# Kernel optimization log

Hardware: AMD Instinct MI355X
Metric: run time of the kernel (lower is better)

The kernel has to match this reference:

```python
import jax, jax.numpy as jnp
import numpy as np
import math

B, S, D_MODEL, H, D_LATENT = 2, 2048, 2048, 16, 512
D_HEAD = D_MODEL // H


def setup_inputs() -> dict:
    key = jax.random.key(0)
    ks = jax.random.split(key, 6)
    s = lambda fan: 1.0 / math.sqrt(fan)
    return {
        "x": jax.random.normal(ks[0], (B, S, D_MODEL), dtype=jnp.float32),
        "W_q": jax.random.normal(ks[1], (D_MODEL, D_MODEL), dtype=jnp.float32) * s(D_MODEL),
        "W_down_kv": jax.random.normal(ks[2], (D_LATENT, D_MODEL), dtype=jnp.float32) * s(D_MODEL),
        "W_up_k": jax.random.normal(ks[3], (H, D_HEAD, D_LATENT), dtype=jnp.float32) * s(D_LATENT),
        "W_up_v": jax.random.normal(ks[4], (H, D_HEAD, D_LATENT), dtype=jnp.float32) * s(D_LATENT),
        "W_o": jax.random.normal(ks[5], (D_MODEL, D_MODEL), dtype=jnp.float32) * s(D_MODEL),
    }


def reference(x, W_q, W_down_kv, W_up_k, W_up_v, W_o):
    b, s_len, d_model = x.shape
    # Q: (B, H, S, Dh)
    Q = (x @ W_q.T).reshape(b, s_len, H, D_HEAD).transpose(0, 2, 1, 3)
    # latent KV: (B, S, d_latent)
    C_kv = x @ W_down_kv.T
    # per-head up-projections fused into one einsum: (B, H, S, Dh)
    K = jnp.einsum("bsl,hdl->bhsd", C_kv, W_up_k)
    V = jnp.einsum("bsl,hdl->bhsd", C_kv, W_up_v)
    scores = jnp.einsum("bhsd,bhtd->bhst", Q, K) / math.sqrt(D_HEAD)
    attn = jax.nn.softmax(scores, axis=-1)  # dropout p=0 / eval -> identity
    out = jnp.einsum("bhst,bhtd->bhsd", attn, V)
    out = out.transpose(0, 2, 1, 3).reshape(b, s_len, H * D_HEAD)
    return out @ W_o.T
```

## Files before the change

kernel.cpp:

```cpp
#include <hip/hip_runtime.h>
#include <hip/hip_bf16.h>

typedef __hip_bfloat16 bf16;
typedef __attribute__((ext_vector_type(8))) short short8v;
typedef __attribute__((ext_vector_type(4))) short short4v;
typedef __attribute__((ext_vector_type(4))) float f32x4;
typedef __attribute__((ext_vector_type(16))) float f32x16;
typedef __attribute__((ext_vector_type(4))) unsigned int uint4v;
typedef unsigned int u32;

#define MFMA_16x16x32(a, b, c) __builtin_amdgcn_mfma_f32_16x16x32_bf16((a), (b), (c), 0, 0, 0)
#define MFMA_32x32x16(a, b, c) __builtin_amdgcn_mfma_f32_32x32x16_bf16((a), (b), (c), 0, 0, 0)

constexpr int Bc = 2, Sc = 2048, DMc = 2048, Hc = 16, DLc = 512, DHc = 128;

__device__ __forceinline__ void gload_lds16(const bf16* g, void* lds) {
  __builtin_amdgcn_global_load_lds(
      (const __attribute__((address_space(1))) void*)g,
      (__attribute__((address_space(3))) void*)lds, 16, 0, 0);
}

__device__ __forceinline__ unsigned short bf16bits(float f) {
  return __builtin_bit_cast(unsigned short, __float2bfloat16(f));
}

struct CvtArgs {
  const float* src[6];
  bf16* dst[6];
  unsigned int cum[6];
  unsigned int total4;
};

__global__ __launch_bounds__(256) void cvt_all_kernel(CvtArgs a)
{
  unsigned int i = blockIdx.x * 256 + threadIdx.x;
  const unsigned int stride = gridDim.x * 256;
  for (; i < a.total4; i += stride) {
    int s = 0;
#pragma unroll
    for (int k = 1; k < 6; ++k) s += (i >= a.cum[k]) ? 1 : 0;
    unsigned int off = (i - a.cum[s]) * 4;
    float4 v = *(const float4*)(a.src[s] + off);
    short4v p;
    p[0] = (short)bf16bits(v.x);
    p[1] = (short)bf16bits(v.y);
    p[2] = (short)bf16bits(v.z);
    p[3] = (short)bf16bits(v.w);
    *(short4v*)(a.dst[s] + off) = p;
  }
}

template<int EPI>
__device__ __forceinline__ void gemm_tile_128(
    const bf16* __restrict__ A, const bf16* __restrict__ BT, void* __restrict__ Cv,
    int K, int ldc, int row0, int col0, bf16* As, bf16* Bs)
{
  const int tid = threadIdx.x;
  const int lane = tid & 63, wid = tid >> 6;
  const int wr = wid >> 1, wc = wid & 1;

  f32x4 acc[4][4] = {};

  const int srow = tid >> 2;
  const int scol = (tid & 3) * 8;
  const bf16* Ag = A + (size_t)(row0 + srow) * K + scol;
  const bf16* Bg = BT + (size_t)(col0 + srow) * K + scol;
  char* AsW = (char*)As + wid * 1024;
  char* BsW = (char*)Bs + wid * 1024;

  const int fr = lane & 15, fk = (lane >> 4) * 8;
  const bf16* aRd = As + (wr * 64 + fr) * 32 + fk;
  const bf16* bRd = Bs + (wc * 64 + fr) * 32 + fk;

  for (int k0 = 0; k0 < K; k0 += 32) {
    gload_lds16(Ag, AsW);
    gload_lds16(Ag + (size_t)64 * K, AsW + 4096);
    gload_lds16(Bg, BsW);
    gload_lds16(Bg + (size_t)64 * K, BsW + 4096);
    Ag += 32; Bg += 32;
    __syncthreads();
    short8v a[4], b[4];
#pragma unroll
    for (int m = 0; m < 4; ++m) a[m] = *(const short8v*)(aRd + m * 16 * 32);
#pragma unroll
    for (int n = 0; n < 4; ++n) b[n] = *(const short8v*)(bRd + n * 16 * 32);
#pragma unroll
    for (int m = 0; m < 4; ++m)
#pragma unroll
      for (int n = 0; n < 4; ++n)
        acc[m][n] = MFMA_16x16x32(a[m], b[n], acc[m][n]);
    __syncthreads();
  }

  const int crow = (lane >> 4) * 4, ccol = lane & 15;
  if (EPI == 0) {
    bf16* C = (bf16*)Cv;
#pragma unroll
    for (int m = 0; m < 4; ++m)
#pragma unroll
      for (int n = 0; n < 4; ++n) {
        bf16* Cp = C + (size_t)(row0 + wr * 64 + m * 16 + crow) * ldc
                     + col0 + wc * 64 + n * 16 + ccol;
#pragma unroll
        for (int r = 0; r < 4; ++r)
          Cp[(size_t)r * ldc] = __float2bfloat16(acc[m][n][r]);
      }
  } else if (EPI == 1) {
    bf16* C = (bf16*)Cv;
#pragma unroll
    for (int m = 0; m < 4; ++m)
#pragma unroll
      for (int n = 0; n < 4; ++n) {
        short4v pk;
#pragma unroll
        for (int r = 0; r < 4; ++r)
          pk[r] = (short)bf16bits(acc[m][n][r]);
        bf16* Cp = C + (size_t)(col0 + wc * 64 + n * 16 + ccol) * ldc
                     + row0 + wr * 64 + m * 16 + crow;
        *(short4v*)Cp = pk;
      }
  } else {
    float* C = (float*)Cv;
#pragma unroll
    for (int m = 0; m < 4; ++m)
#pragma unroll
      for (int n = 0; n < 4; ++n) {
        float* Cp = C + (size_t)(row0 + wr * 64 + m * 16 + crow) * ldc
                      + col0 + wc * 64 + n * 16 + ccol;
#pragma unroll
        for (int r = 0; r < 4; ++r)
          Cp[(size_t)r * ldc] = acc[m][n][r];
      }
  }
}

__device__ __forceinline__ int2 xcd_remap(int nx, int ny) {
  int flat = blockIdx.x + nx * blockIdx.y;
  int chunk = (nx * ny) >> 3;
  int role = (flat & 7) * chunk + (flat >> 3);
  return make_int2(role % nx, role / nx);
}

template<int EPI>
__global__ __launch_bounds__(256) void gemm_bt_kernel(
    const bf16* __restrict__ A, const bf16* __restrict__ BT, void* __restrict__ C,
    int K, int N)
{
  __shared__ bf16 As[128 * 32];
  __shared__ bf16 Bs[128 * 32];
  int2 bb = xcd_remap(gridDim.x, gridDim.y);
  gemm_tile_128<EPI>(A, BT, C, K, N, bb.y * 128, bb.x * 128, As, Bs);
}

__global__ __launch_bounds__(256) void qkv_gemm_kernel(
    const bf16* __restrict__ xb, const bf16* __restrict__ Wqb,
    const bf16* __restrict__ Wdkvb, bf16* __restrict__ Qb, bf16* __restrict__ Ck)
{
  __shared__ bf16 As[128 * 32];
  __shared__ bf16 Bs[128 * 32];
  int2 bb = xcd_remap(20, 32);
  const int bx = bb.x, row0 = bb.y * 128;
  if (bx < 16)
    gemm_tile_128<0>(xb, Wqb, Qb, DMc, DMc, row0, bx * 128, As, Bs);
  else
    gemm_tile_128<0>(xb, Wdkvb, Ck, DMc, DLc, row0, (bx - 16) * 128, As, Bs);
}

#define GPHASE(bufv, KK, MH)                                                \
  do {                                                                      \
    const char* ap_ = aR + (bufv) * 32768 + (KK) * 8192 + (MH) * 4096;      \
    const char* bp_ = bR + (bufv) * 32768 + (KK) * 8192;                    \
    short8v af_[4], bf_[4];                                                 \
    _Pragma("unroll")                                                       \
    for (int m4 = 0; m4 < 4; ++m4)                                          \
      af_[m4] = *(const short8v*)(ap_ + m4 * 1024);                         \
    _Pragma("unroll")                                                       \
    for (int n = 0; n < 4; ++n)                                             \
      bf_[n] = *(const short8v*)(bp_ + n * 1024);                           \
    __builtin_amdgcn_s_setprio(1);                                          \
    _Pragma("unroll")                                                       \
    for (int m4 = 0; m4 < 4; ++m4)                                          \
      _Pragma("unroll")                                                     \
      for (int n = 0; n < 4; ++n)                                           \
        acc[(MH) * 4 + m4][n] =                                             \
            MFMA_16x16x32(af_[m4], bf_[n], acc[(MH) * 4 + m4][n]);          \
    __builtin_amdgcn_s_setprio(0);                                          \
  } while (0)

template<int EPI>
__device__ __forceinline__ void gemm_tile_256(
    const bf16* __restrict__ A, const bf16* __restrict__ BT, void* __restrict__ Cv,
    int K, int ldc, int row0, int col0, char* AsC, char* BsC)
{
  const int tid = threadIdx.x;
  const int lane = tid & 63, wid = tid >> 6;
  const int wm = wid >> 2, wn = wid & 3;
  const int fr = lane & 15, g = lane >> 4;

  f32x4 acc[8][4] = {};

  const int srow = tid >> 2;
  const int scolS = ((tid & 3) * 16) ^ (((srow >> 1) & 3) << 4);
  const bf16* sA = A + (size_t)(row0 + srow) * K + (scolS >> 1);
  const bf16* sB = BT + (size_t)(col0 + srow) * K + (scolS >> 1);
  char* AsW = AsC + wid * 1024;
  char* BsW = BsC + wid * 1024;

  auto ISSA = [&](int buf, int h, int kk, int kt) {
    gload_lds16(sA + (size_t)(h * 128) * K + kt * 64 + kk * 32,
                AsW + buf * 32768 + h * 16384 + kk * 8192);
  };
  auto ISSB = [&](int buf, int h, int kk, int kt) {
    gload_lds16(sB + (size_t)(h * 128) * K + kt * 64 + kk * 32,
                BsW + buf * 32768 + h * 16384 + kk * 8192);
  };

  const int rdLane = fr * 64 + ((g * 16) ^ (((fr >> 1) & 3) << 4));
  const char* aR = AsC + wm * 16384 + rdLane;
  const char* bR = BsC + (wn >> 1) * 16384 + (wn & 1) * 4096 + rdLane;

  ISSA(0, 0, 0, 0); ISSA(0, 1, 0, 0); ISSB(0, 0, 0, 0); ISSB(0, 1, 0, 0);
  ISSA(0, 0, 1, 0); ISSA(0, 1, 1, 0); ISSB(0, 0, 1, 0); ISSB(0, 1, 1, 0);

  const int KT = K >> 6;
  for (int kt = 0; kt < KT - 1; ++kt) {
    const int buf = kt & 1, nb = buf ^ 1;
    asm volatile("s_waitcnt vmcnt(4)" ::: "memory");
    __builtin_amdgcn_s_barrier();
    asm volatile("" ::: "memory");
    ISSA(nb, 0, 0, kt + 1); ISSA(nb, 1, 0, kt + 1);
    GPHASE(buf, 0, 0);
    ISSB(nb, 0, 0, kt + 1); ISSB(nb, 1, 0, kt + 1);
    GPHASE(buf, 0, 1);
    asm volatile("s_waitcnt vmcnt(4)" ::: "memory");
    __builtin_amdgcn_s_barrier();
    asm volatile("" ::: "memory");
    ISSA(nb, 0, 1, kt + 1); ISSA(nb, 1, 1, kt + 1);
    GPHASE(buf, 1, 0);
    ISSB(nb, 0, 1, kt + 1); ISSB(nb, 1, 1, kt + 1);
    GPHASE(buf, 1, 1);
  }
  {
    const int buf = (KT - 1) & 1;
    asm volatile("s_waitcnt vmcnt(4)" ::: "memory");
    __builtin_amdgcn_s_barrier();
    asm volatile("" ::: "memory");
    GPHASE(buf, 0, 0);
    GPHASE(buf, 0, 1);
    asm volatile("s_waitcnt vmcnt(0)" ::: "memory");
    __builtin_amdgcn_s_barrier();
    asm volatile("" ::: "memory");
    GPHASE(buf, 1, 0);
    GPHASE(buf, 1, 1);
  }

  const int crow = g * 4, ccol = fr;
  if (EPI == 0) {
    bf16* C = (bf16*)Cv;
#pragma unroll
    for (int m = 0; m < 8; ++m)
#pragma unroll
      for (int n = 0; n < 4; ++n) {
        bf16* Cp = C + (size_t)(row0 + wm * 128 + m * 16 + crow) * ldc
                     + col0 + wn * 64 + n * 16 + ccol;
#pragma unroll
        for (int r = 0; r < 4; ++r)
          Cp[(size_t)r * ldc] = __float2bfloat16(acc[m][n][r]);
      }
  } else if (EPI == 1) {
    bf16* C = (bf16*)Cv;
#pragma unroll
    for (int m = 0; m < 8; ++m)
#pragma unroll
      for (int n = 0; n < 4; ++n) {
        short4v pk;
#pragma unroll
        for (int r = 0; r < 4; ++r)
          pk[r] = (short)bf16bits(acc[m][n][r]);
        bf16* Cp = C + (size_t)(col0 + wn * 64 + n * 16 + ccol) * ldc
                     + row0 + wm * 128 + m * 16 + crow;
        *(short4v*)Cp = pk;
      }
  } else {
    float* C = (float*)Cv;
#pragma unroll
    for (int m = 0; m < 8; ++m)
#pragma unroll
      for (int n = 0; n < 4; ++n) {
        float* Cp = C + (size_t)(row0 + wm * 128 + m * 16 + crow) * ldc
                      + col0 + wn * 64 + n * 16 + ccol;
#pragma unroll
        for (int r = 0; r < 4; ++r)
          Cp[(size_t)r * ldc] = acc[m][n][r];
      }
  }
}

__global__ __launch_bounds__(512, 2) void up_gemm_kernel(
    const bf16* __restrict__ Ck, const bf16* __restrict__ Wukb,
    const bf16* __restrict__ Wuvb, bf16* __restrict__ Kcat, bf16* __restrict__ VTcat)
{
  __shared__ char As[65536];
  __shared__ char Bs[65536];
  const int flat = blockIdx.x + 16 * blockIdx.y;
  const int role = (flat & 7) * 32 + (flat >> 3);
  const int bx = role & 15, by = role >> 4;
  if (bx < 8)
    gemm_tile_256<0>(Ck, Wukb, Kcat, DLc, DMc, by * 256, bx * 256, As, Bs);
  else
    gemm_tile_256<1>(Ck, Wuvb, VTcat, DLc, Bc * Sc, by * 256, (bx - 8) * 256, As, Bs);
}

constexpr int KVB = 64;
constexpr int NTT = Sc / KVB;
constexpr int VSTR = Bc * Sc;

__global__ __launch_bounds__(256, 2) void mla_attn_kernel(
    const bf16* __restrict__ Q, const bf16* __restrict__ Kcat,
    const bf16* __restrict__ VTcat, bf16* __restrict__ O)
{
  __shared__ bf16 Ks[2][KVB * 128];
  __shared__ bf16 Vs[2][64 * 128];

  const int tid = threadIdx.x, lane = tid & 63, wid = tid >> 6;
  const int l31 = lane & 31, hi = lane >> 5;

  const int flat = blockIdx.x + 16 * (blockIdx.y + 16 * blockIdx.z);
  const int role = (flat & 7) * 64 + (flat >> 3);
  const int qb = role & 15, h = (role >> 4) & 15, b = role >> 8;
  const int q0 = qb * 128 + wid * 32;

  const bf16* Qp = Q + (size_t)(b * Sc + q0 + l31) * DMc + h * DHc + hi * 8;
  short8v qf[8];
#pragma unroll
  for (int kk = 0; kk < 8; ++kk) qf[kk] = *(const short8v*)(Qp + kk * 16);

  const bf16* Kb = Kcat + (size_t)b * Sc * DMc + h * DHc;
  const bf16* Vb = VTcat + (size_t)(h * DHc) * VSTR + b * Sc;

  const int srow = wid * 4 + (lane >> 4);
  const int scolB = (lane & 15) * 16;
  const int swzK0 = ((srow & 7) << 4) ^ (((srow >> 3) & 1) << 6);
  const bf16* kpE = Kb + (size_t)srow * DMc + (((scolB ^ swzK0) & 255) >> 1);
  const bf16* kpO = Kb + (size_t)srow * DMc + ((((scolB ^ swzK0) ^ 128) & 255) >> 1);
  const int swzV0 = ((srow & 7) << 4) ^ (((srow >> 3) & 1) << 7);
  const int vcp = scolB ^ swzV0;
  const bf16* vp = Vb + (size_t)(2 * srow + (vcp >> 7)) * VSTR + ((vcp & 127) >> 1);

  auto STAGE = [&](int buf, int t0) {
    char* kd = (char*)(&Ks[buf][0]) + wid * 1024;
    gload_lds16(kpE + (size_t)t0 * DMc, kd);
    gload_lds16(kpO + (size_t)(t0 + 16) * DMc, kd + 4096);
    gload_lds16(kpE + (size_t)(t0 + 32) * DMc, kd + 8192);
    gload_lds16(kpO + (size_t)(t0 + 48) * DMc, kd + 12288);
    char* vd = (char*)(&Vs[buf][0]) + wid * 1024;
    const bf16* v0 = vp + t0;
    gload_lds16(v0, vd);
    gload_lds16(v0 + (size_t)32 * VSTR, vd + 4096);
    gload_lds16(v0 + (size_t)64 * VSTR, vd + 8192);
    gload_lds16(v0 + (size_t)96 * VSTR, vd + 12288);
  };

  const int swzR = ((l31 & 7) << 4) ^ (((l31 >> 3) & 1) << 6) ^ (((l31 >> 4) & 1) << 7);
  const int swzVR = (((l31 >> 1) & 7) << 4) ^ (((l31 >> 4) & 1) << 7);

  f32x16 oacc[4] = {};
  f32x16 sA0, sA1, sB0, sB1;
  short8v pf[4];
  float m_r = -1e30f, l_r = 0.f, msc = 0.f;
  const float SCL2 = 0.12751650f;
  const float THRraw = 47.0f;

#define QK_STEP(BC, S0, S1)                                                 \
  do {                                                                      \
    const char* Kc_ = (const char*)(&Ks[BC][0]);                            \
    __builtin_amdgcn_s_setprio(1);                                          \
    _Pragma("unroll")                                                       \
    for (int kk = 0; kk < 8; ++kk) {                                        \
      const int cb_ = (kk * 32 + hi * 16) ^ swzR;                           \
      short8v k0_ = *(const short8v*)(Kc_ + l31 * 256 + cb_);               \
      short8v k1_ = *(const short8v*)(Kc_ + (32 + l31) * 256 + cb_);        \
      S0 = MFMA_32x32x16(k0_, qf[kk], S0);                                  \
      S1 = MFMA_32x32x16(k1_, qf[kk], S1);                                  \
    }                                                                       \
    __builtin_amdgcn_s_setprio(0);                                          \
  } while (0)

#define SOFTMAX(S0, S1)                                                     \
  do {                                                                      \
    float pm = (S0)[0];                                                     \
    _Pragma("unroll")                                                       \
    for (int i = 1; i < 16; ++i) pm = fmaxf(pm, (S0)[i]);                   \
    _Pragma("unroll")                                                       \
    for (int i = 0; i < 16; ++i) pm = fmaxf(pm, (S1)[i]);                   \
    if (!__all(pm - m_r <= THRraw)) {                                       \
      float red = fmaxf(pm, __shfl_xor(pm, 32, 64));                        \
      float mnew = fmaxf(m_r, red);                                         \
      float c = exp2f((m_r - mnew) * SCL2);                                 \
      m_r = mnew;                                                           \
      msc = mnew * SCL2;                                                    \
      l_r *= c;                                                             \
      _Pragma("unroll")                                                     \
      for (int db = 0; db < 4; ++db) oacc[db] *= c;                         \
    }                                                                       \
    _Pragma("unroll")                                                       \
    for (int tt = 0; tt < 2; ++tt) {                                        \
      const f32x16& s_ = tt ? (S1) : (S0);                                  \
      _Pragma("unroll")                                                     \
      for (int half = 0; half < 2; ++half) {                                \
        float e0 = exp2f(__builtin_fmaf(s_[half * 8 + 0], SCL2, -msc));     \
        float e1 = exp2f(__builtin_fmaf(s_[half * 8 + 1], SCL2, -msc));     \
        float e2 = exp2f(__builtin_fmaf(s_[half * 8 + 2], SCL2, -msc));     \
        float e3 = exp2f(__builtin_fmaf(s_[half * 8 + 3], SCL2, -msc));     \
        float e4 = exp2f(__builtin_fmaf(s_[half * 8 + 4], SCL2, -msc));     \
        float e5 = exp2f(__builtin_fmaf(s_[half * 8 + 5], SCL2, -msc));     \
        float e6 = exp2f(__builtin_fmaf(s_[half * 8 + 6], SCL2, -msc));     \
        float e7 = exp2f(__builtin_fmaf(s_[half * 8 + 7], SCL2, -msc));     \
        l_r += ((e0 + e1) + (e2 + e3)) + ((e4 + e5) + (e6 + e7));           \
        u32 cA, cB, cC, cD;                                                 \
        asm("v_cvt_pk_bf16_f32 %0, %1, %2" : "=v"(cA) : "v"(e0), "v"(e1));  \
        asm("v_cvt_pk_bf16_f32 %0, %1, %2" : "=v"(cB) : "v"(e2), "v"(e3));  \
        asm("v_cvt_pk_bf16_f32 %0, %1, %2" : "=v"(cC) : "v"(e4), "v"(e5));  \
        asm("v_cvt_pk_bf16_f32 %0, %1, %2" : "=v"(cD) : "v"(e6), "v"(e7));  \
        asm volatile("v_permlane32_swap_b32 %0, %1" : "+v"(cA), "+v"(cC));  \
        asm volatile("v_permlane32_swap_b32 %0, %1" : "+v"(cB), "+v"(cD));  \
        uint4v w;                                                           \
        w[0] = cA; w[1] = cB; w[2] = cC; w[3] = cD;                         \
        pf[tt * 2 + half] = __builtin_bit_cast(short8v, w);                 \
      }                                                                     \
    }                                                                       \
  } while (0)

#define PV_STEP(BC)                                                         \
  do {                                                                      \
    const char* Vc_ = (const char*)(&Vs[BC][0]);                            \
    __builtin_amdgcn_s_setprio(1);                                          \
    _Pragma("unroll")                                                       \
    for (int db = 0; db < 4; ++db) {                                        \
      const int vrow_ = (db * 16 + (l31 >> 1)) * 256;                       \
      _Pragma("unroll")                                                     \
      for (int ts = 0; ts < 4; ++ts) {                                      \
        const int cb_ = ((l31 & 1) * 128 + ts * 32 + hi * 16) ^ swzVR;      \
        short8v vf_ = *(const short8v*)(Vc_ + vrow_ + cb_);                 \
        oacc[db] = MFMA_32x32x16(vf_, pf[ts], oacc[db]);                    \
      }                                                                     \
    }                                                                       \
    __builtin_amdgcn_s_setprio(0);                                          \
  } while (0)

#define AITER(IT, SO0, SO1, SN0, SN1, DOSTAGE)                              \
  do {                                                                      \
    asm volatile("s_waitcnt vmcnt(0)" ::: "memory");                        \
    __builtin_amdgcn_s_barrier();                                           \
    asm volatile("" ::: "memory");                                          \
    SN0 = (f32x16){}; SN1 = (f32x16){};                                     \
    QK_STEP((IT) & 1, SN0, SN1);                                            \
    SOFTMAX(SO0, SO1);                                                      \
    PV_STEP(((IT) - 1) & 1);                                                \
    __builtin_amdgcn_s_barrier();                                           \
    asm volatile("" ::: "memory");                                          \
    if (DOSTAGE) STAGE(((IT) + 1) & 1, ((IT) + 1) * KVB);                   \
    asm volatile("" ::: "memory");                                          \
  } while (0)

  STAGE(0, 0);
  asm volatile("s_waitcnt vmcnt(0)" ::: "memory");
  __builtin_amdgcn_s_barrier();
  asm volatile("" ::: "memory");
  STAGE(1, KVB);
  sA0 = (f32x16){}; sA1 = (f32x16){};
  QK_STEP(0, sA0, sA1);

  for (int p = 0; p < 15; ++p) {
    AITER(2 * p + 1, sA0, sA1, sB0, sB1, 1);
    AITER(2 * p + 2, sB0, sB1, sA0, sA1, 1);
  }
  AITER(31, sA0, sA1, sB0, sB1, 0);
  SOFTMAX(sB0, sB1);
  PV_STEP(1);

#undef AITER
#undef PV_STEP
#undef SOFTMAX
#undef QK_STEP

  float l = l_r + __shfl_xor(l_r, 32, 64);
  float inv = 1.f / l;
  bf16* Op = O + (size_t)(b * Sc + q0 + l31) * DMc + h * DHc + hi * 4;
#pragma unroll
  for (int db = 0; db < 4; ++db) {
#pragma unroll
    for (int rq = 0; rq < 4; ++rq) {
      short4v pk;
#pragma unroll
      for (int r = 0; r < 4; ++r)
        pk[r] = (short)bf16bits(oacc[db][rq * 4 + r] * inv);
      *(short4v*)(Op + db * 32 + rq * 8) = pk;
    }
  }
}

extern "C" void kernel_launch(void* const* d_in, const int* in_sizes, int n_in,
                              void* d_out, int out_size, void* d_ws, size_t ws_size,
                              hipStream_t stream)
{
  const float* x    = (const float*)d_in[0];
  const float* Wq   = (const float*)d_in[1];
  const float* Wdkv = (const float*)d_in[2];
  const float* Wuk  = (const float*)d_in[3];
  const float* Wuv  = (const float*)d_in[4];
  const float* Wo   = (const float*)d_in[5];
  float* out = (float*)d_out;

  char* ws = (char*)d_ws;
  bf16* Qb    = (bf16*)(ws + 0);
  bf16* Kcat  = (bf16*)(ws + 16777216);
  bf16* VTcat = (bf16*)(ws + 33554432);
  bf16* xb    = (bf16*)(ws + 50331648);
  bf16* AO    = (bf16*)(ws + 50331648);
  bf16* Ck    = (bf16*)(ws + 67108864);
  bf16* Wqb   = (bf16*)(ws + 71303168);
  bf16* Wdkvb = (bf16*)(ws + 79691776);
  bf16* Wukb  = (bf16*)(ws + 81788928);
  bf16* Wuvb  = (bf16*)(ws + 83886080);
  bf16* Wob   = (bf16*)(ws + 85983232);

  dim3 blk(256, 1, 1);

  CvtArgs ca;
  ca.src[0] = x;    ca.dst[0] = xb;
  ca.src[1] = Wq;   ca.dst[1] = Wqb;
  ca.src[2] = Wdkv; ca.dst[2] = Wdkvb;
  ca.src[3] = Wuk;  ca.dst[3] = Wukb;
  ca.src[4] = Wuv;  ca.dst[4] = Wuvb;
  ca.src[5] = Wo;   ca.dst[5] = Wob;
  unsigned int n4[6] = { (unsigned)(Bc * Sc * DMc / 4), (unsigned)(DMc * DMc / 4),
                         (unsigned)(DLc * DMc / 4),     (unsigned)(Hc * DHc * DLc / 4),
                         (unsigned)(Hc * DHc * DLc / 4),(unsigned)(DMc * DMc / 4) };
  unsigned int acc = 0;
  for (int i = 0; i < 6; ++i) { ca.cum[i] = acc; acc += n4[i]; }
  ca.total4 = acc;
  cvt_all_kernel<<<2048, blk, 0, stream>>>(ca);

  qkv_gemm_kernel<<<dim3(20, 32), blk, 0, stream>>>(xb, Wqb, Wdkvb, Qb, Ck);

  up_gemm_kernel<<<dim3(16, 16), dim3(512, 1, 1), 0, stream>>>(Ck, Wukb, Wuvb, Kcat, VTcat);

  mla_attn_kernel<<<dim3(Sc / 128, Hc, Bc), dim3(256, 1, 1), 0, stream>>>(
      Qb, Kcat, VTcat, AO);

  gemm_bt_kernel<2><<<dim3(16, 32), blk, 0, stream>>>(AO, Wob, out, DMc, DMc);
}
```

Before: 236.7 us.

## Replace output projection GEMM with 256x128 tiled double-buffered 512-thread kernel

Swaps the 128x128 single-buffered output projection GEMM for a new 256x128 tile kernel with 512 threads, async global-to-LDS loads into double buffers, XOR-swizzled LDS reads and MFMA priority hints. The larger tile gives more reuse per loaded byte and overlaps loads with MFMA work to cut memory stalls. It uses more LDS and registers per block and launches half as many blocks (256), which may lower occupancy or leave some CUs idle.

Result: slower. 243.5 us (+2.9%).

```diff
diff --git a/kernel.cpp b/kernel.cpp
--- a/kernel.cpp
+++ b/kernel.cpp
@@ -141,17 +141,6 @@
   return make_int2(role % nx, role / nx);
 }
 
-template<int EPI>
-__global__ __launch_bounds__(256) void gemm_bt_kernel(
-    const bf16* __restrict__ A, const bf16* __restrict__ BT, void* __restrict__ C,
-    int K, int N)
-{
-  __shared__ bf16 As[128 * 32];
-  __shared__ bf16 Bs[128 * 32];
-  int2 bb = xcd_remap(gridDim.x, gridDim.y);
-  gemm_tile_128<EPI>(A, BT, C, K, N, bb.y * 128, bb.x * 128, As, Bs);
-}
-
 __global__ __launch_bounds__(256) void qkv_gemm_kernel(
     const bf16* __restrict__ xb, const bf16* __restrict__ Wqb,
     const bf16* __restrict__ Wdkvb, bf16* __restrict__ Qb, bf16* __restrict__ Ck)
@@ -309,6 +298,117 @@
     gemm_tile_256<0>(Ck, Wukb, Kcat, DLc, DMc, by * 256, bx * 256, As, Bs);
   else
     gemm_tile_256<1>(Ck, Wuvb, VTcat, DLc, Bc * Sc, by * 256, (bx - 8) * 256, As, Bs);
+}
+
+#define GPHASE_NB(bufv, KK, MH)                                             \
+  do {                                                                      \
+    const char* ap_ = aR + (bufv) * 32768 + (KK) * 8192 + (MH) * 4096;      \
+    const char* bp_ = bR + (bufv) * 16384 + (KK) * 8192;                    \
+    short8v af_[4], bf_[2];                                                 \
+    _Pragma("unroll")                                                       \
+    for (int m4 = 0; m4 < 4; ++m4)                                          \
+      af_[m4] = *(const short8v*)(ap_ + m4 * 1024);                         \
+    _Pragma("unroll")                                                       \
+    for (int n = 0; n < 2; ++n)                                             \
+      bf_[n] = *(const short8v*)(bp_ + n * 1024);                           \
+    __builtin_amdgcn_s_setprio(1);                                          \
+    _Pragma("unroll")                                                       \
+    for (int m4 = 0; m4 < 4; ++m4)                                          \
+      _Pragma("unroll")                                                     \
+      for (int n = 0; n < 2; ++n)                                           \
+        acc[(MH) * 4 + m4][n] =                                             \
+            MFMA_16x16x32(af_[m4], bf_[n], acc[(MH) * 4 + m4][n]);          \
+    __builtin_amdgcn_s_setprio(0);                                          \
+  } while (0)
+
+__device__ __forceinline__ void gemm_tile_256x128_f32(
+    const bf16* __restrict__ A, const bf16* __restrict__ BT, float* __restrict__ C,
+    int K, int ldc, int row0, int col0, char* AsC, char* BsC)
+{
+  const int tid = threadIdx.x;
+  const int lane = tid & 63, wid = tid >> 6;
+  const int wm = wid >> 2, wn = wid & 3;
+  const int fr = lane & 15, g = lane >> 4;
+
+  f32x4 acc[8][2] = {};
+
+  const int srow = tid >> 2;
+  const int scolS = ((tid & 3) * 16) ^ (((srow >> 1) & 3) << 4);
+  const bf16* sA = A + (size_t)(row0 + srow) * K + (scolS >> 1);
+  const bf16* sB = BT + (size_t)(col0 + srow) * K + (scolS >> 1);
+  char* AsW = AsC + wid * 1024;
+  char* BsW = BsC + wid * 1024;
+
+  auto ISSA = [&](int buf, int h, int kk, int kt) {
+    gload_lds16(sA + (size_t)(h * 128) * K + kt * 64 + kk * 32,
+                AsW + buf * 32768 + h * 16384 + kk * 8192);
+  };
+  auto ISSB = [&](int buf, int kk, int kt) {
+    gload_lds16(sB + (size_t)kt * 64 + kk * 32,
+                BsW + buf * 16384 + kk * 8192);
+  };
+
+  const int rdLane = fr * 64 + ((g * 16) ^ (((fr >> 1) & 3) << 4));
+  const char* aR = AsC + wm * 16384 + rdLane;
+  const char* bR = BsC + wn * 2048 + rdLane;
+
+  ISSA(0, 0, 0, 0); ISSA(0, 1, 0, 0); ISSB(0, 0, 0);
+  ISSA(0, 0, 1, 0); ISSA(0, 1, 1, 0); ISSB(0, 1, 0);
+
+  const int KT = K >> 6;
+  for (int kt = 0; kt < KT - 1; ++kt) {
+    const int buf = kt & 1, nb = buf ^ 1;
+    asm volatile("s_waitcnt vmcnt(3)" ::: "memory");
+    __builtin_amdgcn_s_barrier();
+    asm volatile("" ::: "memory");
+    ISSA(nb, 0, 0, kt + 1);
+    GPHASE_NB(buf, 0, 0);
+    ISSA(nb, 1, 0, kt + 1); ISSB(nb, 0, kt + 1);
+    GPHASE_NB(buf, 0, 1);
+    asm volatile("s_waitcnt vmcnt(3)" ::: "memory");
+    __builtin_amdgcn_s_barrier();
+    asm volatile("" ::: "memory");
+    ISSA(nb, 0, 1, kt + 1);
+    GPHASE_NB(buf, 1, 0);
+    ISSA(nb, 1, 1, kt + 1); ISSB(nb, 1, kt + 1);
+    GPHASE_NB(buf, 1, 1);
+  }
+  {
+    const int buf = (KT - 1) & 1;
+    asm volatile("s_waitcnt vmcnt(3)" ::: "memory");
+    __builtin_amdgcn_s_barrier();
+    asm volatile("" ::: "memory");
+    GPHASE_NB(buf, 0, 0);
+    GPHASE_NB(buf, 0, 1);
+    asm volatile("s_waitcnt vmcnt(0)" ::: "memory");
+    __builtin_amdgcn_s_barrier();
+    asm volatile("" ::: "memory");
+    GPHASE_NB(buf, 1, 0);
+    GPHASE_NB(buf, 1, 1);
+  }
+
+  const int crow = g * 4, ccol = fr;
+#pragma unroll
+  for (int m = 0; m < 8; ++m)
+#pragma unroll
+    for (int n = 0; n < 2; ++n) {
+      float* Cp = C + (size_t)(row0 + wm * 128 + m * 16 + crow) * ldc
+                    + col0 + wn * 32 + n * 16 + ccol;
+#pragma unroll
+      for (int r = 0; r < 4; ++r)
+        Cp[(size_t)r * ldc] = acc[m][n][r];
+    }
+}
+
+__global__ __launch_bounds__(512, 2) void out_gemm_kernel(
+    const bf16* __restrict__ AO, const bf16* __restrict__ Wob, float* __restrict__ out)
+{
+  __shared__ char As[65536];
+  __shared__ char Bs[32768];
+  const int flat = blockIdx.x + 16 * blockIdx.y;
+  const int role = (flat & 7) * 32 + (flat >> 3);
+  const int bx = role & 15, by = role >> 4;
+  gemm_tile_256x128_f32(AO, Wob, out, DMc, DMc, by * 256, bx * 128, As, Bs);
 }
 
 constexpr int KVB = 64;
@@ -549,5 +649,5 @@
   mla_attn_kernel<<<dim3(Sc / 128, Hc, Bc), dim3(256, 1, 1), 0, stream>>>(
       Qb, Kcat, VTcat, AO);
 
-  gemm_bt_kernel<2><<<dim3(16, 32), blk, 0, stream>>>(AO, Wob, out, DMc, DMc);
-}
+  out_gemm_kernel<<<dim3(16, 16), dim3(512, 1, 1), 0, stream>>>(AO, Wob, out);
+}
```
